# Kernel tuning notes

Measured on AMD Instinct MI355X. Metric: run time of the kernel, lower is better.

Reference implementation:

```python
import jax, jax.numpy as jnp
import numpy as np

N_LAYERS, K, EPS = 3, 3, 1e-5
N, E, IN_CH, HID, OUT_CH = 50000, 800000, 16, 64, 4


def setup_inputs() -> dict:
    key = jax.random.key(0)
    ks = jax.random.split(key, 10)
    x = jax.random.normal(ks[0], (N, IN_CH), jnp.float32)
    edge_index = jax.random.randint(ks[1], (2, E), 0, N, dtype=jnp.int32)
    batch = jnp.zeros((N,), jnp.int32)  # unused by forward, kept for signature parity
    W_in = jax.random.normal(ks[2], (IN_CH, HID), jnp.float32) / np.sqrt(IN_CH)
    b_in = jnp.zeros((HID,), jnp.float32)
    cheb_W = jax.random.normal(ks[3], (N_LAYERS, K, HID, HID), jnp.float32) / np.sqrt(HID)
    cheb_b = jnp.zeros((N_LAYERS, HID), jnp.float32)
    ln_g = jnp.ones((N_LAYERS, HID), jnp.float32)
    ln_b = jnp.zeros((N_LAYERS, HID), jnp.float32)
    W_out = jax.random.normal(ks[4], (HID, OUT_CH), jnp.float32) / np.sqrt(HID)
    b_out = jnp.zeros((OUT_CH,), jnp.float32)
    return dict(x=x, edge_index=edge_index, batch=batch, W_in=W_in, b_in=b_in,
                cheb_W=cheb_W, cheb_b=cheb_b, ln_g=ln_g, ln_b=ln_b,
                W_out=W_out, b_out=b_out)


def _layernorm(h, g, b):
    mu = h.mean(-1, keepdims=True)
    var = ((h - mu) ** 2).mean(-1, keepdims=True)
    return (h - mu) * jax.lax.rsqrt(var + EPS) * g + b


def reference(x, edge_index, batch, W_in, b_in, cheb_W, cheb_b, ln_g, ln_b, W_out, b_out):
    n = x.shape[0]
    src, dst = edge_index[0], edge_index[1]
    # PyG ChebConv sym norm with lambda_max=2: L_hat = -D^{-1/2} A D^{-1/2}, zero diagonal
    deg = jax.ops.segment_sum(jnp.ones_like(src, x.dtype), src, num_segments=n)
    dinv = jnp.where(deg > 0, 1.0 / jnp.sqrt(jnp.maximum(deg, 1.0)), 0.0)
    w = -dinv[src] * dinv[dst]  # [E]

    def prop(h):  # h: [N, H] -> L_hat @ h via gather/scatter over edges
        return jax.ops.segment_sum(w[:, None] * h[src], dst, num_segments=n)

    h = x @ W_in + b_in
    for i in range(N_LAYERS):
        identity = h
        Tx0 = h
        out = Tx0 @ cheb_W[i, 0]
        Tx1 = prop(Tx0)
        out = out + Tx1 @ cheb_W[i, 1]
        for k in range(2, K):
            Tx2 = 2.0 * prop(Tx1) - Tx0
            out = out + Tx2 @ cheb_W[i, k]
            Tx0, Tx1 = Tx1, Tx2
        h = jax.nn.relu(out + cheb_b[i])  # dropout inactive (eval)
        h = h + identity
        h = _layernorm(h, ln_g[i], ln_b[i])
    return h @ W_out + b_out
```

## Files before the change

kernel.cpp:

```cpp
#include <hip/hip_runtime.h>
#include <hip/hip_bf16.h>

#define HID 64
#define CAP 64
#define LDK 200
#define Q4W 6272
typedef __hip_bfloat16 bf16;
typedef __attribute__((ext_vector_type(8))) short short8x;
typedef __attribute__((ext_vector_type(4))) float f32x4;

__device__ __forceinline__ float ldf(const void* p, int i, int bf) {
    return bf ? __bfloat162float(((const bf16*)p)[i]) : ((const float*)p)[i];
}
__device__ __forceinline__ unsigned short f2u16(float f) {
    bf16 h = __float2bfloat16(f);
    return *(unsigned short*)&h;
}
__device__ __forceinline__ float u162f(unsigned short u) {
    return __bfloat162float(*(const bf16*)&u);
}
__device__ __forceinline__ unsigned int pack2(float a, float b) {
    return (unsigned int)f2u16(a) | ((unsigned int)f2u16(b) << 16);
}
__device__ __forceinline__ void accum8(float* acc, uint4 r) {
    acc[0] += __uint_as_float(r.x << 16);
    acc[1] += __uint_as_float(r.x & 0xffff0000u);
    acc[2] += __uint_as_float(r.y << 16);
    acc[3] += __uint_as_float(r.y & 0xffff0000u);
    acc[4] += __uint_as_float(r.z << 16);
    acc[5] += __uint_as_float(r.z & 0xffff0000u);
    acc[6] += __uint_as_float(r.w << 16);
    acc[7] += __uint_as_float(r.w & 0xffff0000u);
}

__global__ void init_all(const unsigned short* __restrict__ lng, int* __restrict__ flag,
                         bf16* __restrict__ HsPad, bf16* __restrict__ T1sPad) {
    int i = threadIdx.x;
    if (i == 0) *flag = (lng[0] == 0x3F80) ? 1 : 0;
    if (i < HID) {
        HsPad[i] = __float2bfloat16(0.f);
        T1sPad[i] = __float2bfloat16(0.f);
    }
}

__global__ __launch_bounds__(1024) void hist_both(const int* __restrict__ src,
                                                  const int* __restrict__ dst,
                                                  unsigned int* __restrict__ degS,
                                                  unsigned int* __restrict__ degD,
                                                  int E, int Q, int QW) {
    __shared__ unsigned int hs[Q4W];
    __shared__ unsigned int hd[Q4W];
    int q = blockIdx.x & 3, sl = blockIdx.x >> 2;
    for (int i = threadIdx.x; i < QW; i += 1024) { hs[i] = 0u; hd[i] = 0u; }
    __syncthreads();
    int per = (E + 63) >> 6;
    int start = sl * per, end = min(start + per, E);
    int lo = q * Q;
    for (int e = start + threadIdx.x; e < end; e += 1024) {
        int s = src[e] - lo;
        int d = dst[e] - lo;
        if ((unsigned)s < (unsigned)Q) atomicAdd(&hs[s >> 1], (s & 1) ? 0x10000u : 1u);
        if ((unsigned)d < (unsigned)Q) atomicAdd(&hd[d >> 1], (d & 1) ? 0x10000u : 1u);
    }
    __syncthreads();
    unsigned int* os = degS + (size_t)blockIdx.x * QW;
    unsigned int* od = degD + (size_t)blockIdx.x * QW;
    for (int i = threadIdx.x; i < QW; i += 1024) { os[i] = hs[i]; od[i] = hd[i]; }
}

__global__ void prefix_prep(const unsigned int* __restrict__ degS,
                            const unsigned int* __restrict__ degD,
                            unsigned int* __restrict__ prefD,
                            float* __restrict__ dinv, int* __restrict__ cnts,
                            const void* __restrict__ chW, const int* __restrict__ flagp,
                            bf16* __restrict__ WT, int N, int Q, int QW, int dblkW) {
    int bid = blockIdx.x;
    if (bid < dblkW) {
        int wI = bid * 256 + threadIdx.x;
        if (wI < 4 * QW) {
            int q = wI / QW;
            int w = wI - q * QW;
            unsigned int run = 0, ss = 0;
            for (int sl = 0; sl < 64; ++sl) {
                size_t idx = (size_t)(sl * 4 + q) * QW + w;
                prefD[idx] = run;
                run += degD[idx];
                ss += degS[idx];
            }
            int n0 = q * Q + (w << 1);
            int d0 = (int)(ss & 0xffffu), d1 = (int)(ss >> 16);
            if (n0 < N) {
                dinv[n0] = (d0 > 0) ? 1.0f / sqrtf((float)d0) : 0.0f;
                cnts[n0] = (int)(run & 0xffffu);
            }
            if (((w << 1) + 1) < Q && (n0 + 1) < N) {
                dinv[n0 + 1] = (d1 > 0) ? 1.0f / sqrtf((float)d1) : 0.0f;
                cnts[n0 + 1] = (int)(run >> 16);
            }
        }
    } else {
        int bf = *flagp;
        int idx = (bid - dblkW) * 256 + threadIdx.x;
        if (idx < 3 * 64 * 192) {
            int L = idx / (64 * 192);
            int rem = idx % (64 * 192);
            int n = rem / 192;
            int k = rem % 192;
            int mat = k >> 6, r = k & 63;
            float v = ldf(chW, ((L * 3 + mat) * 64 + r) * 64 + n, bf);
            WT[idx] = __float2bfloat16(v);
        }
    }
}

__global__ __launch_bounds__(1024) void fill_prefix(const int* __restrict__ src,
                                                    const int* __restrict__ dst,
                                                    const unsigned int* __restrict__ prefD,
                                                    unsigned short* __restrict__ srcsB,
                                                    int E, int N, int Q, int QW) {
    __shared__ unsigned int loc[Q4W];
    int q = blockIdx.x & 3, sl = blockIdx.x >> 2;
    const unsigned int* bp = prefD + (size_t)(sl * 4 + q) * QW;
    for (int i = threadIdx.x; i < QW; i += 1024) loc[i] = bp[i];
    __syncthreads();
    int per = (E + 63) >> 6;
    int start = sl * per, end = min(start + per, E);
    int lo = q * Q;
    for (int e = start + threadIdx.x; e < end; e += 1024) {
        int d = dst[e] - lo;
        if ((unsigned)d < (unsigned)Q) {
            unsigned int old = atomicAdd(&loc[d >> 1], (d & 1) ? 0x10000u : 1u);
            int slot = (int)((d & 1) ? (old >> 16) : (old & 0xffffu));
            if (slot < CAP) srcsB[(size_t)(lo + d) * CAP + slot] = (unsigned short)src[e];
        }
    }
    if (sl == 63) {
        __syncthreads();
        for (int i = threadIdx.x; i < QW; i += 1024) {
            unsigned int tot2 = loc[i];
            #pragma unroll
            for (int half = 0; half < 2; ++half) {
                int d = (i << 1) + half;
                int n = lo + d;
                unsigned int tot = (half ? (tot2 >> 16) : tot2) & 0xffffu;
                if (d < Q && n < N) {
                    int pe = min((int)((tot + 7u) & ~7u), CAP);
                    for (int s2 = (int)tot; s2 < pe; ++s2)
                        srcsB[(size_t)n * CAP + s2] = (unsigned short)N;
                }
            }
        }
    }
}

__global__ __launch_bounds__(256) void input_proj(const void* __restrict__ x,
                                                  const void* __restrict__ Win,
                                                  const void* __restrict__ bin,
                                                  const float* __restrict__ dinv,
                                                  const int* __restrict__ flagp,
                                                  bf16* __restrict__ H,
                                                  bf16* __restrict__ Hs, int N) {
    int bf = *flagp;
    __shared__ float w[16 * HID];
    __shared__ float bb[HID];
    for (int i = threadIdx.x; i < 16 * HID; i += 256) w[i] = ldf(Win, i, bf);
    if (threadIdx.x < HID) bb[threadIdx.x] = ldf(bin, threadIdx.x, bf);
    __syncthreads();
    int t = blockIdx.x * 256 + threadIdx.x;
    int n = t >> 6, j = t & 63;
    if (n >= N) return;
    float acc = bb[j];
    #pragma unroll
    for (int k = 0; k < 16; ++k) acc += ldf(x, n * 16 + k, bf) * w[k * HID + j];
    float dv = dinv[n];
    H[(size_t)n * HID + j] = __float2bfloat16(acc);
    Hs[(size_t)n * HID + j] = __float2bfloat16(acc * dv);
}

__global__ __launch_bounds__(256) void prop8(const int* __restrict__ cnts,
                                             const unsigned short* __restrict__ srcsB,
                                             const float* __restrict__ dinv,
                                             const bf16* __restrict__ Hs,
                                             bf16* __restrict__ Tout,
                                             bf16* __restrict__ Touts,
                                             int N, int writeScaled) {
    int n = blockIdx.x * 4 + (threadIdx.x >> 6);
    if (n >= N) return;
    int lane = threadIdx.x & 63;
    int sv = srcsB[n * CAP + lane];
    int cnt = min(cnts[n], CAP);
    int groups = (cnt + 7) >> 3;
    int sub = lane & 7, g8 = lane >> 3;
    const unsigned short* HsU = (const unsigned short*)Hs;
    float acc[8] = {0.f, 0.f, 0.f, 0.f, 0.f, 0.f, 0.f, 0.f};
    int g = 0;
    for (; g + 2 <= groups; g += 2) {
        int s0 = __shfl(sv, g * 8 + g8, 64);
        int s1 = __shfl(sv, g * 8 + 8 + g8, 64);
        uint4 r0 = *(const uint4*)(HsU + (size_t)s0 * HID + sub * 8);
        uint4 r1 = *(const uint4*)(HsU + (size_t)s1 * HID + sub * 8);
        accum8(acc, r0);
        accum8(acc, r1);
    }
    if (g < groups) {
        int s0 = __shfl(sv, g * 8 + g8, 64);
        uint4 r0 = *(const uint4*)(HsU + (size_t)s0 * HID + sub * 8);
        accum8(acc, r0);
    }
    #pragma unroll
    for (int m = 8; m < 64; m <<= 1) {
        #pragma unroll
        for (int k = 0; k < 8; ++k) acc[k] += __shfl_xor(acc[k], m, 64);
    }
    if (g8 == 0) {
        float dv = dinv[n];
        float t[8];
        #pragma unroll
        for (int k = 0; k < 8; ++k) t[k] = -dv * acc[k];
        uint4 o;
        o.x = pack2(t[0], t[1]); o.y = pack2(t[2], t[3]);
        o.z = pack2(t[4], t[5]); o.w = pack2(t[6], t[7]);
        *(uint4*)((unsigned short*)Tout + (size_t)n * HID + sub * 8) = o;
        if (writeScaled) {
            uint4 os;
            os.x = pack2(t[0] * dv, t[1] * dv); os.y = pack2(t[2] * dv, t[3] * dv);
            os.z = pack2(t[4] * dv, t[5] * dv); os.w = pack2(t[6] * dv, t[7] * dv);
            *(uint4*)((unsigned short*)Touts + (size_t)n * HID + sub * 8) = os;
        }
    }
}

__global__ __launch_bounds__(256) void fused_layer_mfma(
    bf16* __restrict__ H, bf16* __restrict__ Hs,
    const bf16* __restrict__ T1, const bf16* __restrict__ T2,
    const bf16* __restrict__ WT, const float* __restrict__ dinv,
    const void* __restrict__ cb, const void* __restrict__ g, const void* __restrict__ b,
    int voff, const int* __restrict__ flagp, int N, int ntiles,
    const void* __restrict__ Wout, const void* __restrict__ bout,
    void* __restrict__ yout, int lastL) {
    int bf = *flagp;
    __shared__ unsigned short Bs[64 * LDK];
    __shared__ unsigned short As[16 * LDK];
    __shared__ float red[4][4][4][2];
    __shared__ float woLds[HID * 4];
    __shared__ float boLds[4];
    int tid = threadIdx.x;
    const unsigned int* WT32 = (const unsigned int*)WT;
    for (int i = tid; i < 64 * 96; i += 256) {
        int row = i / 96, c2 = i % 96;
        *(unsigned int*)&Bs[row * LDK + c2 * 2] = WT32[i];
    }
    if (lastL) {
        for (int i = tid; i < HID * 4; i += 256) woLds[i] = ldf(Wout, i, bf);
        if (tid < 4) boLds[tid] = ldf(bout, tid, bf);
    }
    int w = tid >> 6, lane = tid & 63;
    int q = lane >> 4, c = lane & 15;
    int ncol = w * 16 + c;
    float cbv = ldf(cb, voff + ncol, bf);
    float gv  = ldf(g,  voff + ncol, bf);
    float bv  = ldf(b,  voff + ncol, bf);
    int srow = tid >> 4, scg = tid & 15;
    __syncthreads();

    for (int t = blockIdx.x; t < ntiles; t += gridDim.x) {
        int base = t * 16;
        int node = base + srow;
        uint2 hz = {0u, 0u}, t1z = {0u, 0u}, t2z = {0u, 0u};
        if (node < N) {
            size_t off = (size_t)node * HID + scg * 4;
            hz  = *(const uint2*)((const unsigned short*)H + off);
            t1z = *(const uint2*)((const unsigned short*)T1 + off);
            t2z = *(const uint2*)((const unsigned short*)T2 + off);
        }
        float h0 = __uint_as_float(hz.x << 16), h1 = __uint_as_float(hz.x & 0xffff0000u);
        float h2 = __uint_as_float(hz.y << 16), h3 = __uint_as_float(hz.y & 0xffff0000u);
        float u0 = __uint_as_float(t2z.x << 16), u1 = __uint_as_float(t2z.x & 0xffff0000u);
        float u2 = __uint_as_float(t2z.y << 16), u3 = __uint_as_float(t2z.y & 0xffff0000u);
        uint2 t3z;
        t3z.x = pack2(2.f * u0 - h0, 2.f * u1 - h1);
        t3z.y = pack2(2.f * u2 - h2, 2.f * u3 - h3);
        unsigned short* Arow = &As[srow * LDK + scg * 4];
        *(uint2*)(Arow)        = hz;
        *(uint2*)(Arow + 64)   = t1z;
        *(uint2*)(Arow + 128)  = t3z;
        __syncthreads();

        f32x4 acc = {0.f, 0.f, 0.f, 0.f};
        #pragma unroll
        for (int kk = 0; kk < 6; ++kk) {
            int kb = kk * 32 + q * 8;
            short8x af = *(const short8x*)&As[c * LDK + kb];
            short8x bfv = *(const short8x*)&Bs[ncol * LDK + kb];
            acc = __builtin_amdgcn_mfma_f32_16x16x32_bf16(af, bfv, acc, 0, 0, 0);
        }

        float v[4], ps[4], ps2[4];
        #pragma unroll
        for (int r = 0; r < 4; ++r) {
            int m = q * 4 + r;
            float hval = u162f(As[m * LDK + ncol]);
            float o = acc[r] + cbv;
            v[r] = fmaxf(o, 0.f) + hval;
            ps[r] = v[r];
            ps2[r] = v[r] * v[r];
            #pragma unroll
            for (int msk = 1; msk < 16; msk <<= 1) {
                ps[r]  += __shfl_xor(ps[r],  msk, 64);
                ps2[r] += __shfl_xor(ps2[r], msk, 64);
            }
        }
        if (c == 0) {
            #pragma unroll
            for (int r = 0; r < 4; ++r) {
                red[w][q][r][0] = ps[r];
                red[w][q][r][1] = ps2[r];
            }
        }
        __syncthreads();
        #pragma unroll
        for (int r = 0; r < 4; ++r) {
            float S  = red[0][q][r][0] + red[1][q][r][0] + red[2][q][r][0] + red[3][q][r][0];
            float S2 = red[0][q][r][1] + red[1][q][r][1] + red[2][q][r][1] + red[3][q][r][1];
            float mu = S * (1.f / 64.f);
            float var = S2 * (1.f / 64.f) - mu * mu;
            float hn = (v[r] - mu) * rsqrtf(var + 1e-5f) * gv + bv;
            int nd = base + q * 4 + r;
            if (!lastL) {
                if (nd < N) {
                    float dvn = dinv[nd];
                    H[(size_t)nd * HID + ncol] = __float2bfloat16(hn);
                    Hs[(size_t)nd * HID + ncol] = __float2bfloat16(hn * dvn);
                }
            } else {
                As[(q * 4 + r) * LDK + ncol] = f2u16((nd < N) ? hn : 0.f);
            }
        }
        if (lastL) {
            __syncthreads();
            if (w == 0) {
                int m = lane >> 2, j = lane & 3;
                float a = boLds[j];
                #pragma unroll
                for (int k = 0; k < HID; ++k)
                    a += u162f(As[m * LDK + k]) * woLds[k * 4 + j];
                int nd = base + m;
                if (nd < N) {
                    if (bf) ((unsigned short*)yout)[(size_t)nd * 4 + j] = f2u16(a);
                    else    ((float*)yout)[(size_t)nd * 4 + j] = a;
                }
            }
        }
        __syncthreads();
    }
}

extern "C" void kernel_launch(void* const* d_in, const int* in_sizes, int n_in,
                              void* d_out, int out_size, void* d_ws, size_t ws_size,
                              hipStream_t stream) {
    const void* x    = d_in[0];
    const int*  ei   = (const int*)d_in[1];
    const void* Win  = d_in[3];
    const void* bin  = d_in[4];
    const void* chW  = d_in[5];
    const void* chb  = d_in[6];
    const void* lng  = d_in[7];
    const void* lnb  = d_in[8];
    const void* Wout = d_in[9];
    const void* bout = d_in[10];

    int N = in_sizes[0] / 16;
    int E = in_sizes[1] / 2;
    const int* src = ei;
    const int* dst = ei + E;
    int ntiles = (N + 15) / 16;
    int Q = (N + 3) / 4;
    int QW = (Q + 1) / 2;
    int dblkW = (4 * QW + 255) / 256;

    char* p = (char*)d_ws;
    auto carve = [&](size_t bytes) {
        char* r = p;
        p += (bytes + 255) & ~(size_t)255;
        return r;
    };
    int*            flag  = (int*)carve(256);
    float*          dinv  = (float*)carve((size_t)N * 4);
    int*            cnts  = (int*)carve((size_t)N * 4);
    unsigned short* srcsB = (unsigned short*)carve((size_t)N * CAP * 2);
    bf16*           WT    = (bf16*)carve((size_t)3 * 64 * 192 * 2);
    bf16*           H     = (bf16*)carve((size_t)N * HID * 2);
    bf16*           Hs    = (bf16*)carve((size_t)(N + 1) * HID * 2);
    bf16*           T1    = (bf16*)carve((size_t)N * HID * 2);
    bf16*           T1s   = (bf16*)carve((size_t)(N + 1) * HID * 2);
    bf16*           T2    = (bf16*)carve((size_t)N * HID * 2);
    unsigned int*   degS  = (unsigned int*)carve((size_t)256 * QW * 4);
    unsigned int*   degD  = (unsigned int*)carve((size_t)256 * QW * 4);
    unsigned int*   prefD = (unsigned int*)carve((size_t)256 * QW * 4);

    hipLaunchKernelGGL(init_all, dim3(1), dim3(256), 0, stream,
                       (const unsigned short*)lng, flag,
                       Hs + (size_t)N * HID, T1s + (size_t)N * HID);
    hipLaunchKernelGGL(hist_both, dim3(256), dim3(1024), 0, stream,
                       src, dst, degS, degD, E, Q, QW);
    hipLaunchKernelGGL(prefix_prep, dim3(dblkW + 144), dim3(256), 0, stream,
                       degS, degD, prefD, dinv, cnts, chW, flag, WT, N, Q, QW, dblkW);
    hipLaunchKernelGGL(fill_prefix, dim3(256), dim3(1024), 0, stream,
                       src, dst, prefD, srcsB, E, N, Q, QW);
    hipLaunchKernelGGL(input_proj, dim3((N * 64 + 255) / 256), dim3(256), 0, stream,
                       x, Win, bin, dinv, flag, H, Hs, N);

    for (int L = 0; L < 3; ++L) {
        hipLaunchKernelGGL(prop8, dim3((N + 3) / 4), dim3(256), 0, stream,
                           cnts, srcsB, dinv, Hs, T1, T1s, N, 1);
        hipLaunchKernelGGL(prop8, dim3((N + 3) / 4), dim3(256), 0, stream,
                           cnts, srcsB, dinv, T1s, T2, (bf16*)0, N, 0);
        hipLaunchKernelGGL(fused_layer_mfma, dim3(1024), dim3(256), 0, stream,
                           H, Hs, T1, T2, WT + (size_t)L * 64 * 192, dinv,
                           chb, lng, lnb, L * HID, flag, N, ntiles,
                           Wout, bout, d_out, (L == 2) ? 1 : 0);
    }
}
```

Before: 308.5 us.

## Fuse second propagation into layer MFMA kernel and merge setup kernels

The second Chebyshev propagation (gather over T1s) now runs inside the fused layer kernel, and its result is written straight into shared memory instead of a global T2 buffer. This removes one launch per layer and the T2 write/read round trip. init_all is folded into hist_both, and fill_prefix and input_proj are merged into one launch. The cost is that the fused layer kernel now also carries the gather work, done by 4 waves per 16-row tile with a less unrolled gather loop, which may lower memory-level parallelism. The merge of fill_prefix and input_proj assumes input_proj reads dinv and flag produced by earlier kernels, and does not depend on srcsB, so running both in one launch is safe.

```diff
diff --git a/kernel.cpp b/kernel.cpp
--- a/kernel.cpp
+++ b/kernel.cpp
@@ -33,23 +33,24 @@
     acc[7] += __uint_as_float(r.w & 0xffff0000u);
 }
 
-__global__ void init_all(const unsigned short* __restrict__ lng, int* __restrict__ flag,
-                         bf16* __restrict__ HsPad, bf16* __restrict__ T1sPad) {
-    int i = threadIdx.x;
-    if (i == 0) *flag = (lng[0] == 0x3F80) ? 1 : 0;
-    if (i < HID) {
-        HsPad[i] = __float2bfloat16(0.f);
-        T1sPad[i] = __float2bfloat16(0.f);
-    }
-}
-
 __global__ __launch_bounds__(1024) void hist_both(const int* __restrict__ src,
                                                   const int* __restrict__ dst,
                                                   unsigned int* __restrict__ degS,
                                                   unsigned int* __restrict__ degD,
-                                                  int E, int Q, int QW) {
+                                                  int E, int Q, int QW,
+                                                  const unsigned short* __restrict__ lng,
+                                                  int* __restrict__ flag,
+                                                  bf16* __restrict__ HsPad,
+                                                  bf16* __restrict__ T1sPad) {
     __shared__ unsigned int hs[Q4W];
     __shared__ unsigned int hd[Q4W];
+    if (blockIdx.x == 0) {
+        if (threadIdx.x == 0) *flag = (lng[0] == 0x3F80) ? 1 : 0;
+        if (threadIdx.x < HID) {
+            HsPad[threadIdx.x] = __float2bfloat16(0.f);
+            T1sPad[threadIdx.x] = __float2bfloat16(0.f);
+        }
+    }
     int q = blockIdx.x & 3, sl = blockIdx.x >> 2;
     for (int i = threadIdx.x; i < QW; i += 1024) { hs[i] = 0u; hd[i] = 0u; }
     __syncthreads();
@@ -113,68 +114,64 @@
     }
 }
 
-__global__ __launch_bounds__(1024) void fill_prefix(const int* __restrict__ src,
-                                                    const int* __restrict__ dst,
-                                                    const unsigned int* __restrict__ prefD,
-                                                    unsigned short* __restrict__ srcsB,
-                                                    int E, int N, int Q, int QW) {
+__global__ __launch_bounds__(1024) void fill_input(
+    const int* __restrict__ src, const int* __restrict__ dst,
+    const unsigned int* __restrict__ prefD, unsigned short* __restrict__ srcsB,
+    int E, int N, int Q, int QW,
+    const void* __restrict__ x, const void* __restrict__ Win,
+    const void* __restrict__ bin, const float* __restrict__ dinv,
+    const int* __restrict__ flagp, bf16* __restrict__ H, bf16* __restrict__ Hs) {
     __shared__ unsigned int loc[Q4W];
-    int q = blockIdx.x & 3, sl = blockIdx.x >> 2;
-    const unsigned int* bp = prefD + (size_t)(sl * 4 + q) * QW;
-    for (int i = threadIdx.x; i < QW; i += 1024) loc[i] = bp[i];
-    __syncthreads();
-    int per = (E + 63) >> 6;
-    int start = sl * per, end = min(start + per, E);
-    int lo = q * Q;
-    for (int e = start + threadIdx.x; e < end; e += 1024) {
-        int d = dst[e] - lo;
-        if ((unsigned)d < (unsigned)Q) {
-            unsigned int old = atomicAdd(&loc[d >> 1], (d & 1) ? 0x10000u : 1u);
-            int slot = (int)((d & 1) ? (old >> 16) : (old & 0xffffu));
-            if (slot < CAP) srcsB[(size_t)(lo + d) * CAP + slot] = (unsigned short)src[e];
-        }
-    }
-    if (sl == 63) {
-        __syncthreads();
-        for (int i = threadIdx.x; i < QW; i += 1024) {
-            unsigned int tot2 = loc[i];
-            #pragma unroll
-            for (int half = 0; half < 2; ++half) {
-                int d = (i << 1) + half;
-                int n = lo + d;
-                unsigned int tot = (half ? (tot2 >> 16) : tot2) & 0xffffu;
-                if (d < Q && n < N) {
-                    int pe = min((int)((tot + 7u) & ~7u), CAP);
-                    for (int s2 = (int)tot; s2 < pe; ++s2)
-                        srcsB[(size_t)n * CAP + s2] = (unsigned short)N;
-                }
-            }
-        }
-    }
-}
-
-__global__ __launch_bounds__(256) void input_proj(const void* __restrict__ x,
-                                                  const void* __restrict__ Win,
-                                                  const void* __restrict__ bin,
-                                                  const float* __restrict__ dinv,
-                                                  const int* __restrict__ flagp,
-                                                  bf16* __restrict__ H,
-                                                  bf16* __restrict__ Hs, int N) {
-    int bf = *flagp;
-    __shared__ float w[16 * HID];
+    __shared__ float wsh[16 * HID];
     __shared__ float bb[HID];
-    for (int i = threadIdx.x; i < 16 * HID; i += 256) w[i] = ldf(Win, i, bf);
-    if (threadIdx.x < HID) bb[threadIdx.x] = ldf(bin, threadIdx.x, bf);
-    __syncthreads();
-    int t = blockIdx.x * 256 + threadIdx.x;
-    int n = t >> 6, j = t & 63;
-    if (n >= N) return;
-    float acc = bb[j];
-    #pragma unroll
-    for (int k = 0; k < 16; ++k) acc += ldf(x, n * 16 + k, bf) * w[k * HID + j];
-    float dv = dinv[n];
-    H[(size_t)n * HID + j] = __float2bfloat16(acc);
-    Hs[(size_t)n * HID + j] = __float2bfloat16(acc * dv);
+    if (blockIdx.x < 256) {
+        int q = blockIdx.x & 3, sl = blockIdx.x >> 2;
+        const unsigned int* bp = prefD + (size_t)(sl * 4 + q) * QW;
+        for (int i = threadIdx.x; i < QW; i += 1024) loc[i] = bp[i];
+        __syncthreads();
+        int per = (E + 63) >> 6;
+        int start = sl * per, end = min(start + per, E);
+        int lo = q * Q;
+        for (int e = start + threadIdx.x; e < end; e += 1024) {
+            int d = dst[e] - lo;
+            if ((unsigned)d < (unsigned)Q) {
+                unsigned int old = atomicAdd(&loc[d >> 1], (d & 1) ? 0x10000u : 1u);
+                int slot = (int)((d & 1) ? (old >> 16) : (old & 0xffffu));
+                if (slot < CAP) srcsB[(size_t)(lo + d) * CAP + slot] = (unsigned short)src[e];
+            }
+        }
+        if (sl == 63) {
+            __syncthreads();
+            for (int i = threadIdx.x; i < QW; i += 1024) {
+                unsigned int tot2 = loc[i];
+                #pragma unroll
+                for (int half = 0; half < 2; ++half) {
+                    int d = (i << 1) + half;
+                    int n = lo + d;
+                    unsigned int tot = (half ? (tot2 >> 16) : tot2) & 0xffffu;
+                    if (d < Q && n < N) {
+                        int pe = min((int)((tot + 7u) & ~7u), CAP);
+                        for (int s2 = (int)tot; s2 < pe; ++s2)
+                            srcsB[(size_t)n * CAP + s2] = (unsigned short)N;
+                    }
+                }
+            }
+        }
+    } else {
+        int bf = *flagp;
+        for (int i = threadIdx.x; i < 16 * HID; i += 1024) wsh[i] = ldf(Win, i, bf);
+        if (threadIdx.x < HID) bb[threadIdx.x] = ldf(bin, threadIdx.x, bf);
+        __syncthreads();
+        int t = (blockIdx.x - 256) * 1024 + threadIdx.x;
+        int n = t >> 6, j = t & 63;
+        if (n >= N) return;
+        float acc = bb[j];
+        #pragma unroll
+        for (int k = 0; k < 16; ++k) acc += ldf(x, n * 16 + k, bf) * wsh[k * HID + j];
+        float dv = dinv[n];
+        H[(size_t)n * HID + j] = __float2bfloat16(acc);
+        Hs[(size_t)n * HID + j] = __float2bfloat16(acc * dv);
+    }
 }
 
 __global__ __launch_bounds__(256) void prop8(const int* __restrict__ cnts,
@@ -182,8 +179,7 @@
                                              const float* __restrict__ dinv,
                                              const bf16* __restrict__ Hs,
                                              bf16* __restrict__ Tout,
-                                             bf16* __restrict__ Touts,
-                                             int N, int writeScaled) {
+                                             bf16* __restrict__ Touts, int N) {
     int n = blockIdx.x * 4 + (threadIdx.x >> 6);
     if (n >= N) return;
     int lane = threadIdx.x & 63;
@@ -221,18 +217,17 @@
         o.x = pack2(t[0], t[1]); o.y = pack2(t[2], t[3]);
         o.z = pack2(t[4], t[5]); o.w = pack2(t[6], t[7]);
         *(uint4*)((unsigned short*)Tout + (size_t)n * HID + sub * 8) = o;
-        if (writeScaled) {
-            uint4 os;
-            os.x = pack2(t[0] * dv, t[1] * dv); os.y = pack2(t[2] * dv, t[3] * dv);
-            os.z = pack2(t[4] * dv, t[5] * dv); os.w = pack2(t[6] * dv, t[7] * dv);
-            *(uint4*)((unsigned short*)Touts + (size_t)n * HID + sub * 8) = os;
-        }
+        uint4 os;
+        os.x = pack2(t[0] * dv, t[1] * dv); os.y = pack2(t[2] * dv, t[3] * dv);
+        os.z = pack2(t[4] * dv, t[5] * dv); os.w = pack2(t[6] * dv, t[7] * dv);
+        *(uint4*)((unsigned short*)Touts + (size_t)n * HID + sub * 8) = os;
     }
 }
 
 __global__ __launch_bounds__(256) void fused_layer_mfma(
     bf16* __restrict__ H, bf16* __restrict__ Hs,
-    const bf16* __restrict__ T1, const bf16* __restrict__ T2,
+    const bf16* __restrict__ T1, const bf16* __restrict__ T1s,
+    const int* __restrict__ cnts, const unsigned short* __restrict__ srcsB,
     const bf16* __restrict__ WT, const float* __restrict__ dinv,
     const void* __restrict__ cb, const void* __restrict__ g, const void* __restrict__ b,
     int voff, const int* __restrict__ flagp, int N, int ntiles,
@@ -261,18 +256,57 @@
     float gv  = ldf(g,  voff + ncol, bf);
     float bv  = ldf(b,  voff + ncol, bf);
     int srow = tid >> 4, scg = tid & 15;
+    int sub = lane & 7, g8 = lane >> 3;
+    const unsigned short* TsU = (const unsigned short*)T1s;
     __syncthreads();
 
     for (int t = blockIdx.x; t < ntiles; t += gridDim.x) {
         int base = t * 16;
+
+        #pragma unroll
+        for (int i = 0; i < 4; ++i) {
+            int nloc = (w << 2) + i;
+            int n = base + nloc;
+            if (n < N) {
+                int sv = srcsB[(size_t)n * CAP + lane];
+                int cnt = min(cnts[n], CAP);
+                int groups = (cnt + 7) >> 3;
+                float acc2[8] = {0.f, 0.f, 0.f, 0.f, 0.f, 0.f, 0.f, 0.f};
+                for (int gg = 0; gg < groups; ++gg) {
+                    int s0 = __shfl(sv, gg * 8 + g8, 64);
+                    uint4 r0 = *(const uint4*)(TsU + (size_t)s0 * HID + sub * 8);
+                    accum8(acc2, r0);
+                }
+                #pragma unroll
+                for (int m = 8; m < 64; m <<= 1) {
+                    #pragma unroll
+                    for (int k = 0; k < 8; ++k) acc2[k] += __shfl_xor(acc2[k], m, 64);
+                }
+                float dv = dinv[n];
+                if (g8 == 0) {
+                    uint4 o;
+                    o.x = pack2(-dv * acc2[0], -dv * acc2[1]);
+                    o.y = pack2(-dv * acc2[2], -dv * acc2[3]);
+                    o.z = pack2(-dv * acc2[4], -dv * acc2[5]);
+                    o.w = pack2(-dv * acc2[6], -dv * acc2[7]);
+                    *(uint4*)&As[nloc * LDK + 128 + sub * 8] = o;
+                }
+            } else if (g8 == 0) {
+                uint4 z = {0u, 0u, 0u, 0u};
+                *(uint4*)&As[nloc * LDK + 128 + sub * 8] = z;
+            }
+        }
+        __syncthreads();
+
         int node = base + srow;
-        uint2 hz = {0u, 0u}, t1z = {0u, 0u}, t2z = {0u, 0u};
+        uint2 hz = {0u, 0u}, t1z = {0u, 0u};
         if (node < N) {
             size_t off = (size_t)node * HID + scg * 4;
             hz  = *(const uint2*)((const unsigned short*)H + off);
             t1z = *(const uint2*)((const unsigned short*)T1 + off);
-            t2z = *(const uint2*)((const unsigned short*)T2 + off);
-        }
+        }
+        unsigned short* Arow = &As[srow * LDK + scg * 4];
+        uint2 t2z = *(const uint2*)(Arow + 128);
         float h0 = __uint_as_float(hz.x << 16), h1 = __uint_as_float(hz.x & 0xffff0000u);
         float h2 = __uint_as_float(hz.y << 16), h3 = __uint_as_float(hz.y & 0xffff0000u);
         float u0 = __uint_as_float(t2z.x << 16), u1 = __uint_as_float(t2z.x & 0xffff0000u);
@@ -280,7 +314,6 @@
         uint2 t3z;
         t3z.x = pack2(2.f * u0 - h0, 2.f * u1 - h1);
         t3z.y = pack2(2.f * u2 - h2, 2.f * u3 - h3);
-        unsigned short* Arow = &As[srow * LDK + scg * 4];
         *(uint2*)(Arow)        = hz;
         *(uint2*)(Arow + 64)   = t1z;
         *(uint2*)(Arow + 128)  = t3z;
@@ -377,6 +410,7 @@
     int Q = (N + 3) / 4;
     int QW = (Q + 1) / 2;
     int dblkW = (4 * QW + 255) / 256;
+    int inBlocks = (N * 64 + 1023) / 1024;
 
     char* p = (char*)d_ws;
     auto carve = [&](size_t bytes) {
@@ -393,30 +427,26 @@
     bf16*           Hs    = (bf16*)carve((size_t)(N + 1) * HID * 2);
     bf16*           T1    = (bf16*)carve((size_t)N * HID * 2);
     bf16*           T1s   = (bf16*)carve((size_t)(N + 1) * HID * 2);
-    bf16*           T2    = (bf16*)carve((size_t)N * HID * 2);
     unsigned int*   degS  = (unsigned int*)carve((size_t)256 * QW * 4);
     unsigned int*   degD  = (unsigned int*)carve((size_t)256 * QW * 4);
     unsigned int*   prefD = (unsigned int*)carve((size_t)256 * QW * 4);
 
-    hipLaunchKernelGGL(init_all, dim3(1), dim3(256), 0, stream,
+    hipLaunchKernelGGL(hist_both, dim3(256), dim3(1024), 0, stream,
+                       src, dst, degS, degD, E, Q, QW,
                        (const unsigned short*)lng, flag,
                        Hs + (size_t)N * HID, T1s + (size_t)N * HID);
-    hipLaunchKernelGGL(hist_both, dim3(256), dim3(1024), 0, stream,
-                       src, dst, degS, degD, E, Q, QW);
     hipLaunchKernelGGL(prefix_prep, dim3(dblkW + 144), dim3(256), 0, stream,
                        degS, degD, prefD, dinv, cnts, chW, flag, WT, N, Q, QW, dblkW);
-    hipLaunchKernelGGL(fill_prefix, dim3(256), dim3(1024), 0, stream,
-                       src, dst, prefD, srcsB, E, N, Q, QW);
-    hipLaunchKernelGGL(input_proj, dim3((N * 64 + 255) / 256), dim3(256), 0, stream,
-                       x, Win, bin, dinv, flag, H, Hs, N);
+    hipLaunchKernelGGL(fill_input, dim3(256 + inBlocks), dim3(1024), 0, stream,
+                       src, dst, prefD, srcsB, E, N, Q, QW,
+                       x, Win, bin, dinv, flag, H, Hs);
 
     for (int L = 0; L < 3; ++L) {
         hipLaunchKernelGGL(prop8, dim3((N + 3) / 4), dim3(256), 0, stream,
-                           cnts, srcsB, dinv, Hs, T1, T1s, N, 1);
-        hipLaunchKernelGGL(prop8, dim3((N + 3) / 4), dim3(256), 0, stream,
-                           cnts, srcsB, dinv, T1s, T2, (bf16*)0, N, 0);
+                           cnts, srcsB, dinv, Hs, T1, T1s, N);
         hipLaunchKernelGGL(fused_layer_mfma, dim3(1024), dim3(256), 0, stream,
-                           H, Hs, T1, T2, WT + (size_t)L * 64 * 192, dinv,
+                           H, Hs, T1, T1s, cnts, srcsB,
+                           WT + (size_t)L * 64 * 192, dinv,
                            chb, lng, lnb, L * HID, flag, N, ntiles,
                            Wout, bout, d_out, (L == 2) ? 1 : 0);
     }
```

Measured after the change: 321.8 us. 1.04x slower.
